# Kernel optimization log

Hardware: AMD Instinct MI355X
Metric: run time of the kernel (lower is better)

Reference implementation:

```python
import jax, jax.numpy as jnp
import numpy as np

N, E, D, L = 50000, 600000, 128, 4
SCALE = 0.05  # small init so 4 sum-aggregation layers with residuals stay bounded


def setup_inputs() -> dict:
    key = jax.random.key(0)
    ks = jax.random.split(key, 6)
    x = jax.random.normal(ks[0], (N, D), dtype=jnp.float32)
    edge_index = jax.random.randint(ks[1], (2, E), 0, N, dtype=jnp.int64)
    Wn = jax.random.normal(ks[2], (L, D, D), dtype=jnp.float32) * SCALE
    Wr = jax.random.normal(ks[3], (L, D, D), dtype=jnp.float32) * SCALE
    b = jnp.zeros((L, D), dtype=jnp.float32)
    fcW = jax.random.normal(ks[4], (D, 1), dtype=jnp.float32) * SCALE
    fcb = jnp.zeros((1,), dtype=jnp.float32)
    return {"x": x, "edge_index": edge_index, "Wn": Wn, "Wr": Wr, "b": b,
            "fcW": fcW, "fcb": fcb}


def reference(x, edge_index, Wn, Wr, b, fcW, fcb):
    # AFGCN forward (eval mode: dropout is identity).
    # GraphConv (PyG, aggr='add'): out = sum_{j in N(i)} h_j @ Wn + h_i @ Wr + b
    src, dst = edge_index[0], edge_index[1]
    h0 = x
    h = x
    for l in range(L):
        agg = jax.ops.segment_sum(h[src], dst, num_segments=N)  # [N, D]
        h = jax.nn.relu(agg @ Wn[l] + h @ Wr[l] + b[l])
        h = h + h0  # residual to the input features
    return (h @ fcW + fcb).squeeze(-1)  # [N]
```

## Files before the change

kernel.cpp:

```cpp
#include <hip/hip_runtime.h>


#define D 128

using bf16x8 = __attribute__((ext_vector_type(8))) short;
using f32x4  = __attribute__((ext_vector_type(4))) float;

__device__ inline unsigned short f2b(float f) {
    union { float f; unsigned int u; } v; v.f = f;
    unsigned int u = v.u;
    u += 0x7fffu + ((u >> 16) & 1u);
    return (unsigned short)(u >> 16);
}
__device__ inline float b2f_lo(unsigned int u) { return __uint_as_float(u << 16); }
__device__ inline float b2f_hi(unsigned int u) { return __uint_as_float(u & 0xffff0000u); }

__global__ void k_zero_i32(int* __restrict__ p, int n) {
    int i = blockIdx.x * blockDim.x + threadIdx.x;
    if (i < n) p[i] = 0;
}

__global__ void k_hist(const int* __restrict__ dst, int* __restrict__ cnt, int e) {
    int i = blockIdx.x * blockDim.x + threadIdx.x;
    if (i < e) atomicAdd(&cnt[dst[i]], 1);
}

__global__ __launch_bounds__(256) void k_scan_a(const int* __restrict__ cnt,
                                                int* __restrict__ ro,
                                                int* __restrict__ bsum, int n) {
    __shared__ int s[256];
    int tid = threadIdx.x;
    int base = blockIdx.x * 1024 + tid * 4;
    int c[4];
    #pragma unroll
    for (int k = 0; k < 4; ++k) c[k] = (base + k < n) ? cnt[base + k] : 0;
    s[tid] = c[0] + c[1] + c[2] + c[3];
    __syncthreads();
    #pragma unroll
    for (int off = 1; off < 256; off <<= 1) {
        int add = (tid >= off) ? s[tid - off] : 0;
        __syncthreads();
        s[tid] += add;
        __syncthreads();
    }
    int run = (tid == 0) ? 0 : s[tid - 1];
    #pragma unroll
    for (int k = 0; k < 4; ++k) {
        if (base + k < n) ro[base + k] = run;
        run += c[k];
    }
    if (tid == 255) bsum[blockIdx.x] = s[255];
}

__global__ __launch_bounds__(64) void k_scan_b(int* __restrict__ bsum,
                                               int* __restrict__ ro, int nb, int n) {
    int tid = threadIdx.x;
    int orig = (tid < nb) ? bsum[tid] : 0;
    int v = orig;
    #pragma unroll
    for (int off = 1; off < 64; off <<= 1) {
        int u = __shfl_up(v, off, 64);
        if (tid >= off) v += u;
    }
    if (tid < nb) bsum[tid] = v - orig;
    if (tid == 63) ro[n] = v;
}

__global__ __launch_bounds__(256) void k_scan_c(int* __restrict__ ro,
                                                int* __restrict__ cur,
                                                const int* __restrict__ bsum, int n) {
    int base = blockIdx.x * 1024 + threadIdx.x * 4;
    int off = bsum[blockIdx.x];
    #pragma unroll
    for (int k = 0; k < 4; ++k) {
        int i = base + k;
        if (i < n) { int v = ro[i] + off; ro[i] = v; cur[i] = v; }
    }
}

__global__ void k_scatter(const int* __restrict__ src, const int* __restrict__ dst,
                          int* __restrict__ cur, int* __restrict__ ssrc, int e) {
    int i = blockIdx.x * blockDim.x + threadIdx.x;
    if (i < e) {
        int pos = atomicAdd(&cur[dst[i]], 1);
        ssrc[pos] = src[i];
    }
}

__global__ void k_cvt(const float* __restrict__ in, unsigned short* __restrict__ out,
                      int n8) {
    int i = blockIdx.x * blockDim.x + threadIdx.x;
    if (i >= n8) return;
    float4 a = ((const float4*)in)[i * 2];
    float4 b = ((const float4*)in)[i * 2 + 1];
    ushort4 o0, o1;
    o0.x = f2b(a.x); o0.y = f2b(a.y); o0.z = f2b(a.z); o0.w = f2b(a.w);
    o1.x = f2b(b.x); o1.y = f2b(b.y); o1.z = f2b(b.z); o1.w = f2b(b.w);
    ((ushort4*)out)[i * 2] = o0;
    ((ushort4*)out)[i * 2 + 1] = o1;
}

__global__ void k_pack_B(const float* __restrict__ Wn, const float* __restrict__ Wr,
                         unsigned short* __restrict__ Bp) {
    int t = blockIdx.x * blockDim.x + threadIdx.x;
    int lane = t & 63;
    int nb = (t >> 6) & 7;
    int ks = (t >> 9) & 7;
    int l  = t >> 12;
    int ncol = nb * 16 + (lane & 15);
    int k0 = ks * 32 + (lane >> 4) * 8;
    ushort4 lo, hi;
    unsigned short v[8];
    #pragma unroll
    for (int j = 0; j < 8; ++j) {
        int k = k0 + j;
        float f = (k < D) ? Wn[(size_t)l * D * D + k * D + ncol]
                          : Wr[(size_t)l * D * D + (k - D) * D + ncol];
        v[j] = f2b(f);
    }
    lo.x = v[0]; lo.y = v[1]; lo.z = v[2]; lo.w = v[3];
    hi.x = v[4]; hi.y = v[5]; hi.z = v[6]; hi.w = v[7];
    ((ushort4*)Bp)[t * 2] = lo;
    ((ushort4*)Bp)[t * 2 + 1] = hi;
}

template<bool LAST>
__global__ __launch_bounds__(256) void k_fused(
        const unsigned short* __restrict__ hb,
        const int* __restrict__ ro,
        const int* __restrict__ ssrc,
        const unsigned short* __restrict__ Bp,
        const float* __restrict__ bias,
        const float* __restrict__ x0,
        unsigned short* __restrict__ hb_out,
        const float* __restrict__ fcW,
        const float* __restrict__ fcb,
        float* __restrict__ out, int n) {
    __shared__ unsigned short tsh[4][16][132];
    int wid = threadIdx.x >> 6;
    int lane = threadIdx.x & 63;
    int row0 = (blockIdx.x * 4 + wid) * 16;
    if (row0 >= n) return;

    int r = lane & 15;
    int g = lane >> 4;
    int row = row0 + r;

    float agg[4][8];
    #pragma unroll
    for (int ks = 0; ks < 4; ++ks)
        #pragma unroll
        for (int t = 0; t < 8; ++t) agg[ks][t] = 0.f;

    int s = ro[row], e = ro[row + 1];
    const unsigned short* hbg = hb + g * 8;
    for (int j = s; j < e; ++j) {
        const unsigned short* srcp = hbg + (size_t)ssrc[j] * D;
        uint4 v0 = *(const uint4*)(srcp);
        uint4 v1 = *(const uint4*)(srcp + 32);
        uint4 v2 = *(const uint4*)(srcp + 64);
        uint4 v3 = *(const uint4*)(srcp + 96);
        agg[0][0] += b2f_lo(v0.x); agg[0][1] += b2f_hi(v0.x);
        agg[0][2] += b2f_lo(v0.y); agg[0][3] += b2f_hi(v0.y);
        agg[0][4] += b2f_lo(v0.z); agg[0][5] += b2f_hi(v0.z);
        agg[0][6] += b2f_lo(v0.w); agg[0][7] += b2f_hi(v0.w);
        agg[1][0] += b2f_lo(v1.x); agg[1][1] += b2f_hi(v1.x);
        agg[1][2] += b2f_lo(v1.y); agg[1][3] += b2f_hi(v1.y);
        agg[1][4] += b2f_lo(v1.z); agg[1][5] += b2f_hi(v1.z);
        agg[1][6] += b2f_lo(v1.w); agg[1][7] += b2f_hi(v1.w);
        agg[2][0] += b2f_lo(v2.x); agg[2][1] += b2f_hi(v2.x);
        agg[2][2] += b2f_lo(v2.y); agg[2][3] += b2f_hi(v2.y);
        agg[2][4] += b2f_lo(v2.z); agg[2][5] += b2f_hi(v2.z);
        agg[2][6] += b2f_lo(v2.w); agg[2][7] += b2f_hi(v2.w);
        agg[3][0] += b2f_lo(v3.x); agg[3][1] += b2f_hi(v3.x);
        agg[3][2] += b2f_lo(v3.y); agg[3][3] += b2f_hi(v3.y);
        agg[3][4] += b2f_lo(v3.z); agg[3][5] += b2f_hi(v3.z);
        agg[3][6] += b2f_lo(v3.w); agg[3][7] += b2f_hi(v3.w);
    }

    f32x4 acc[8];
    #pragma unroll
    for (int i = 0; i < 8; ++i) {
        acc[i][0] = 0.f; acc[i][1] = 0.f; acc[i][2] = 0.f; acc[i][3] = 0.f;
    }
    const bf16x8* bp = (const bf16x8*)Bp;

    #pragma unroll
    for (int ks = 0; ks < 4; ++ks) {
        unsigned short af[8];
        #pragma unroll
        for (int t = 0; t < 8; ++t) af[t] = f2b(agg[ks][t]);
        bf16x8 afrag = *(const bf16x8*)af;
        #pragma unroll
        for (int nb = 0; nb < 8; ++nb) {
            bf16x8 bfrag = bp[(ks * 8 + nb) * 64 + lane];
            acc[nb] = __builtin_amdgcn_mfma_f32_16x16x32_bf16(afrag, bfrag, acc[nb], 0, 0, 0);
        }
    }
    const unsigned short* hrow = hb + (size_t)row * D;
    #pragma unroll
    for (int ks = 4; ks < 8; ++ks) {
        bf16x8 afrag = *(const bf16x8*)(hrow + (ks - 4) * 32 + g * 8);
        #pragma unroll
        for (int nb = 0; nb < 8; ++nb) {
            bf16x8 bfrag = bp[(ks * 8 + nb) * 64 + lane];
            acc[nb] = __builtin_amdgcn_mfma_f32_16x16x32_bf16(afrag, bfrag, acc[nb], 0, 0, 0);
        }
    }

    if (!LAST) {
        #pragma unroll
        for (int nb = 0; nb < 8; ++nb) {
            int col = nb * 16 + r;
            float bc = bias[col];
            #pragma unroll
            for (int reg = 0; reg < 4; ++reg) {
                int rowc = row0 + g * 4 + reg;
                float xv = x0[(size_t)rowc * D + col];
                float hv = fmaxf(acc[nb][reg] + bc, 0.f) + xv;
                tsh[wid][g * 4 + reg][col] = f2b(hv);
            }
        }
        #pragma unroll
        for (int it = 0; it < 4; ++it) {
            int rr = it * 4 + g;
            uint4 v = *(const uint4*)&tsh[wid][rr][r * 8];
            *(uint4*)(hb_out + (size_t)(row0 + rr) * D + r * 8) = v;
        }
    } else {
        float p[4] = {0.f, 0.f, 0.f, 0.f};
        #pragma unroll
        for (int nb = 0; nb < 8; ++nb) {
            int col = nb * 16 + r;
            float bc = bias[col];
            float fw = fcW[col];
            #pragma unroll
            for (int reg = 0; reg < 4; ++reg) {
                int rowc = row0 + g * 4 + reg;
                float xv = x0[(size_t)rowc * D + col];
                p[reg] += (fmaxf(acc[nb][reg] + bc, 0.f) + xv) * fw;
            }
        }
        #pragma unroll
        for (int reg = 0; reg < 4; ++reg) {
            #pragma unroll
            for (int m = 1; m < 16; m <<= 1) p[reg] += __shfl_xor(p[reg], m, 64);
        }
        if (r == 0) {
            float fb = fcb[0];
            #pragma unroll
            for (int reg = 0; reg < 4; ++reg) out[row0 + g * 4 + reg] = p[reg] + fb;
        }
    }
}

extern "C" void kernel_launch(void* const* d_in, const int* in_sizes, int n_in,
                              void* d_out, int out_size, void* d_ws, size_t ws_size,
                              hipStream_t stream) {
    const float* x    = (const float*)d_in[0];
    const int*   ei   = (const int*)d_in[1];
    const float* Wn   = (const float*)d_in[2];
    const float* Wr   = (const float*)d_in[3];
    const float* bias = (const float*)d_in[4];
    const float* fcW  = (const float*)d_in[5];
    const float* fcb  = (const float*)d_in[6];
    float* out = (float*)d_out;

    const int n = in_sizes[0] / D;
    const int e = in_sizes[1] / 2;

    const int* src = ei;
    const int* dst = ei + e;

    char* ws = (char*)d_ws;
    unsigned short* xb   = (unsigned short*)ws;  ws += (size_t)n * D * 2;
    unsigned short* hb_a = (unsigned short*)ws;  ws += (size_t)n * D * 2;
    unsigned short* hb_b = (unsigned short*)ws;  ws += (size_t)n * D * 2;
    unsigned short* Bp   = (unsigned short*)ws;  ws += (size_t)4 * 8 * 8 * 64 * 8 * 2;
    int* ro   = (int*)ws;  ws += (size_t)(n + 1) * 4;
    int* cur  = (int*)ws;  ws += (size_t)n * 4;
    int* ssrc = (int*)ws;  ws += (size_t)e * 4;
    int* bsum = (int*)ws;  ws += 256 * 4;
    (void)ws_size;

    const int nscan = (n + 1023) / 1024;

    k_zero_i32<<<(n + 255) / 256, 256, 0, stream>>>(cur, n);
    k_hist<<<(e + 255) / 256, 256, 0, stream>>>(dst, cur, e);
    k_scan_a<<<nscan, 256, 0, stream>>>(cur, ro, bsum, n);
    k_scan_b<<<1, 64, 0, stream>>>(bsum, ro, nscan, n);
    k_scan_c<<<nscan, 256, 0, stream>>>(ro, cur, bsum, n);
    k_scatter<<<(e + 255) / 256, 256, 0, stream>>>(src, dst, cur, ssrc, e);

    int n8 = n * D / 8;
    k_cvt<<<(n8 + 255) / 256, 256, 0, stream>>>(x, xb, n8);
    k_pack_B<<<(4 * 8 * 8 * 64) / 256, 256, 0, stream>>>(Wn, Wr, Bp);

    const int layer_blocks = ((n + 15) / 16 + 3) / 4;
    const size_t bpl = (size_t)8 * 8 * 64 * 8;

    k_fused<false><<<layer_blocks, 256, 0, stream>>>(xb, ro, ssrc, Bp,
            bias, x, hb_a, fcW, fcb, out, n);
    k_fused<false><<<layer_blocks, 256, 0, stream>>>(hb_a, ro, ssrc, Bp + bpl,
            bias + D, x, hb_b, fcW, fcb, out, n);
    k_fused<false><<<layer_blocks, 256, 0, stream>>>(hb_b, ro, ssrc, Bp + 2 * bpl,
            bias + 2 * D, x, hb_a, fcW, fcb, out, n);
    k_fused<true><<<layer_blocks, 256, 0, stream>>>(hb_a, ro, ssrc, Bp + 3 * bpl,
            bias + 3 * D, x, hb_b, fcW, fcb, out, n);
}
```

Before: 249.6 us.

## Sort nodes by degree for load balance, unroll gather, read residual as bf16

```diff
diff --git a/kernel.cpp b/kernel.cpp
--- a/kernel.cpp
+++ b/kernel.cpp
@@ -14,6 +14,11 @@
 }
 __device__ inline float b2f_lo(unsigned int u) { return __uint_as_float(u << 16); }
 __device__ inline float b2f_hi(unsigned int u) { return __uint_as_float(u & 0xffff0000u); }
+__device__ inline unsigned int badd2(unsigned int a, unsigned int b) {
+    unsigned short lo = f2b(b2f_lo(a) + b2f_lo(b));
+    unsigned short hi = f2b(b2f_hi(a) + b2f_hi(b));
+    return (unsigned int)lo | ((unsigned int)hi << 16);
+}
 
 __global__ void k_zero_i32(int* __restrict__ p, int n) {
     int i = blockIdx.x * blockDim.x + threadIdx.x;
@@ -84,6 +89,37 @@
     if (i < e) {
         int pos = atomicAdd(&cur[dst[i]], 1);
         ssrc[pos] = src[i];
+    }
+}
+
+__global__ void k_deg_hist(const int* __restrict__ ro, int* __restrict__ bh, int n) {
+    int i = blockIdx.x * blockDim.x + threadIdx.x;
+    if (i < n) {
+        int d = min(ro[i + 1] - ro[i], 63);
+        atomicAdd(&bh[d], 1);
+    }
+}
+
+__global__ __launch_bounds__(64) void k_bin_scan(const int* __restrict__ bh,
+                                                 int* __restrict__ bcur) {
+    int t = threadIdx.x;
+    int h = bh[t];
+    int v = h;
+    #pragma unroll
+    for (int off = 1; off < 64; off <<= 1) {
+        int u = __shfl_down(v, off, 64);
+        if (t + off < 64) v += u;
+    }
+    bcur[t] = v - h;
+}
+
+__global__ void k_bin_scatter(const int* __restrict__ ro, int* __restrict__ bcur,
+                              int* __restrict__ perm, int n) {
+    int i = blockIdx.x * blockDim.x + threadIdx.x;
+    if (i < n) {
+        int d = min(ro[i + 1] - ro[i], 63);
+        int pos = atomicAdd(&bcur[d], 1);
+        perm[pos] = i;
     }
 }
 
@@ -124,14 +160,21 @@
     ((ushort4*)Bp)[t * 2 + 1] = hi;
 }
 
+#define ACC8(V, KS) do { \
+    agg[KS][0] += b2f_lo((V).x); agg[KS][1] += b2f_hi((V).x); \
+    agg[KS][2] += b2f_lo((V).y); agg[KS][3] += b2f_hi((V).y); \
+    agg[KS][4] += b2f_lo((V).z); agg[KS][5] += b2f_hi((V).z); \
+    agg[KS][6] += b2f_lo((V).w); agg[KS][7] += b2f_hi((V).w); } while (0)
+
 template<bool LAST>
 __global__ __launch_bounds__(256) void k_fused(
         const unsigned short* __restrict__ hb,
         const int* __restrict__ ro,
         const int* __restrict__ ssrc,
+        const int* __restrict__ perm,
         const unsigned short* __restrict__ Bp,
         const float* __restrict__ bias,
-        const float* __restrict__ x0,
+        const unsigned short* __restrict__ xb,
         unsigned short* __restrict__ hb_out,
         const float* __restrict__ fcW,
         const float* __restrict__ fcb,
@@ -144,7 +187,7 @@
 
     int r = lane & 15;
     int g = lane >> 4;
-    int row = row0 + r;
+    int prow = perm[row0 + r];
 
     float agg[4][8];
     #pragma unroll
@@ -152,30 +195,42 @@
         #pragma unroll
         for (int t = 0; t < 8; ++t) agg[ks][t] = 0.f;
 
-    int s = ro[row], e = ro[row + 1];
+    int s = ro[prow], e = ro[prow + 1];
     const unsigned short* hbg = hb + g * 8;
-    for (int j = s; j < e; ++j) {
-        const unsigned short* srcp = hbg + (size_t)ssrc[j] * D;
-        uint4 v0 = *(const uint4*)(srcp);
-        uint4 v1 = *(const uint4*)(srcp + 32);
-        uint4 v2 = *(const uint4*)(srcp + 64);
-        uint4 v3 = *(const uint4*)(srcp + 96);
-        agg[0][0] += b2f_lo(v0.x); agg[0][1] += b2f_hi(v0.x);
-        agg[0][2] += b2f_lo(v0.y); agg[0][3] += b2f_hi(v0.y);
-        agg[0][4] += b2f_lo(v0.z); agg[0][5] += b2f_hi(v0.z);
-        agg[0][6] += b2f_lo(v0.w); agg[0][7] += b2f_hi(v0.w);
-        agg[1][0] += b2f_lo(v1.x); agg[1][1] += b2f_hi(v1.x);
-        agg[1][2] += b2f_lo(v1.y); agg[1][3] += b2f_hi(v1.y);
-        agg[1][4] += b2f_lo(v1.z); agg[1][5] += b2f_hi(v1.z);
-        agg[1][6] += b2f_lo(v1.w); agg[1][7] += b2f_hi(v1.w);
-        agg[2][0] += b2f_lo(v2.x); agg[2][1] += b2f_hi(v2.x);
-        agg[2][2] += b2f_lo(v2.y); agg[2][3] += b2f_hi(v2.y);
-        agg[2][4] += b2f_lo(v2.z); agg[2][5] += b2f_hi(v2.z);
-        agg[2][6] += b2f_lo(v2.w); agg[2][7] += b2f_hi(v2.w);
-        agg[3][0] += b2f_lo(v3.x); agg[3][1] += b2f_hi(v3.x);
-        agg[3][2] += b2f_lo(v3.y); agg[3][3] += b2f_hi(v3.y);
-        agg[3][4] += b2f_lo(v3.z); agg[3][5] += b2f_hi(v3.z);
-        agg[3][6] += b2f_lo(v3.w); agg[3][7] += b2f_hi(v3.w);
+    int j = s;
+    for (; j + 3 < e; j += 4) {
+        const unsigned short* p0 = hbg + (size_t)ssrc[j] * D;
+        const unsigned short* p1 = hbg + (size_t)ssrc[j + 1] * D;
+        const unsigned short* p2 = hbg + (size_t)ssrc[j + 2] * D;
+        const unsigned short* p3 = hbg + (size_t)ssrc[j + 3] * D;
+        uint4 a0 = *(const uint4*)(p0);
+        uint4 a1 = *(const uint4*)(p0 + 32);
+        uint4 a2 = *(const uint4*)(p0 + 64);
+        uint4 a3 = *(const uint4*)(p0 + 96);
+        uint4 b0 = *(const uint4*)(p1);
+        uint4 b1 = *(const uint4*)(p1 + 32);
+        uint4 b2 = *(const uint4*)(p1 + 64);
+        uint4 b3 = *(const uint4*)(p1 + 96);
+        uint4 c0 = *(const uint4*)(p2);
+        uint4 c1 = *(const uint4*)(p2 + 32);
+        uint4 c2 = *(const uint4*)(p2 + 64);
+        uint4 c3 = *(const uint4*)(p2 + 96);
+        uint4 d0 = *(const uint4*)(p3);
+        uint4 d1 = *(const uint4*)(p3 + 32);
+        uint4 d2 = *(const uint4*)(p3 + 64);
+        uint4 d3 = *(const uint4*)(p3 + 96);
+        ACC8(a0, 0); ACC8(a1, 1); ACC8(a2, 2); ACC8(a3, 3);
+        ACC8(b0, 0); ACC8(b1, 1); ACC8(b2, 2); ACC8(b3, 3);
+        ACC8(c0, 0); ACC8(c1, 1); ACC8(c2, 2); ACC8(c3, 3);
+        ACC8(d0, 0); ACC8(d1, 1); ACC8(d2, 2); ACC8(d3, 3);
+    }
+    for (; j < e; ++j) {
+        const unsigned short* p0 = hbg + (size_t)ssrc[j] * D;
+        uint4 a0 = *(const uint4*)(p0);
+        uint4 a1 = *(const uint4*)(p0 + 32);
+        uint4 a2 = *(const uint4*)(p0 + 64);
+        uint4 a3 = *(const uint4*)(p0 + 96);
+        ACC8(a0, 0); ACC8(a1, 1); ACC8(a2, 2); ACC8(a3, 3);
     }
 
     f32x4 acc[8];
@@ -197,7 +252,7 @@
             acc[nb] = __builtin_amdgcn_mfma_f32_16x16x32_bf16(afrag, bfrag, acc[nb], 0, 0, 0);
         }
     }
-    const unsigned short* hrow = hb + (size_t)row * D;
+    const unsigned short* hrow = hb + (size_t)prow * D;
     #pragma unroll
     for (int ks = 4; ks < 8; ++ks) {
         bf16x8 afrag = *(const bf16x8*)(hrow + (ks - 4) * 32 + g * 8);
@@ -208,48 +263,53 @@
         }
     }
 
+    #pragma unroll
+    for (int nb = 0; nb < 8; ++nb) {
+        int col = nb * 16 + r;
+        float bc = bias[col];
+        #pragma unroll
+        for (int reg = 0; reg < 4; ++reg) {
+            tsh[wid][g * 4 + reg][col] = f2b(fmaxf(acc[nb][reg] + bc, 0.f));
+        }
+    }
+
     if (!LAST) {
-        #pragma unroll
-        for (int nb = 0; nb < 8; ++nb) {
-            int col = nb * 16 + r;
-            float bc = bias[col];
-            #pragma unroll
-            for (int reg = 0; reg < 4; ++reg) {
-                int rowc = row0 + g * 4 + reg;
-                float xv = x0[(size_t)rowc * D + col];
-                float hv = fmaxf(acc[nb][reg] + bc, 0.f) + xv;
-                tsh[wid][g * 4 + reg][col] = f2b(hv);
-            }
-        }
         #pragma unroll
         for (int it = 0; it < 4; ++it) {
             int rr = it * 4 + g;
-            uint4 v = *(const uint4*)&tsh[wid][rr][r * 8];
-            *(uint4*)(hb_out + (size_t)(row0 + rr) * D + r * 8) = v;
+            int orow = perm[row0 + rr];
+            uint4 tv = *(const uint4*)&tsh[wid][rr][r * 8];
+            uint4 xv = *(const uint4*)(xb + (size_t)orow * D + r * 8);
+            uint4 o;
+            o.x = badd2(tv.x, xv.x);
+            o.y = badd2(tv.y, xv.y);
+            o.z = badd2(tv.z, xv.z);
+            o.w = badd2(tv.w, xv.w);
+            *(uint4*)(hb_out + (size_t)orow * D + r * 8) = o;
         }
     } else {
-        float p[4] = {0.f, 0.f, 0.f, 0.f};
-        #pragma unroll
-        for (int nb = 0; nb < 8; ++nb) {
-            int col = nb * 16 + r;
-            float bc = bias[col];
-            float fw = fcW[col];
+        float fw8[8];
+        *(float4*)&fw8[0] = *(const float4*)&fcW[r * 8];
+        *(float4*)&fw8[4] = *(const float4*)&fcW[r * 8 + 4];
+        float fb = fcb[0];
+        #pragma unroll
+        for (int it = 0; it < 4; ++it) {
+            int rr = it * 4 + g;
+            int orow = perm[row0 + rr];
+            uint4 tv = *(const uint4*)&tsh[wid][rr][r * 8];
+            uint4 xv = *(const uint4*)(xb + (size_t)orow * D + r * 8);
+            float p;
+            p  = (b2f_lo(tv.x) + b2f_lo(xv.x)) * fw8[0];
+            p += (b2f_hi(tv.x) + b2f_hi(xv.x)) * fw8[1];
+            p += (b2f_lo(tv.y) + b2f_lo(xv.y)) * fw8[2];
+            p += (b2f_hi(tv.y) + b2f_hi(xv.y)) * fw8[3];
+            p += (b2f_lo(tv.z) + b2f_lo(xv.z)) * fw8[4];
+            p += (b2f_hi(tv.z) + b2f_hi(xv.z)) * fw8[5];
+            p += (b2f_lo(tv.w) + b2f_lo(xv.w)) * fw8[6];
+            p += (b2f_hi(tv.w) + b2f_hi(xv.w)) * fw8[7];
             #pragma unroll
-            for (int reg = 0; reg < 4; ++reg) {
-                int rowc = row0 + g * 4 + reg;
-                float xv = x0[(size_t)rowc * D + col];
-                p[reg] += (fmaxf(acc[nb][reg] + bc, 0.f) + xv) * fw;
-            }
-        }
-        #pragma unroll
-        for (int reg = 0; reg < 4; ++reg) {
-            #pragma unroll
-            for (int m = 1; m < 16; m <<= 1) p[reg] += __shfl_xor(p[reg], m, 64);
-        }
-        if (r == 0) {
-            float fb = fcb[0];
-            #pragma unroll
-            for (int reg = 0; reg < 4; ++reg) out[row0 + g * 4 + reg] = p[reg] + fb;
+            for (int m = 1; m < 16; m <<= 1) p += __shfl_xor(p, m, 64);
+            if (r == 0) out[orow] = p + fb;
         }
     }
 }
@@ -281,6 +341,9 @@
     int* cur  = (int*)ws;  ws += (size_t)n * 4;
     int* ssrc = (int*)ws;  ws += (size_t)e * 4;
     int* bsum = (int*)ws;  ws += 256 * 4;
+    int* perm = (int*)ws;  ws += (size_t)n * 4;
+    int* bh   = (int*)ws;  ws += 64 * 4;
+    int* bcur = (int*)ws;  ws += 64 * 4;
     (void)ws_size;
 
     const int nscan = (n + 1023) / 1024;
@@ -292,6 +355,11 @@
     k_scan_c<<<nscan, 256, 0, stream>>>(ro, cur, bsum, n);
     k_scatter<<<(e + 255) / 256, 256, 0, stream>>>(src, dst, cur, ssrc, e);
 
+    k_zero_i32<<<1, 64, 0, stream>>>(bh, 64);
+    k_deg_hist<<<(n + 255) / 256, 256, 0, stream>>>(ro, bh, n);
+    k_bin_scan<<<1, 64, 0, stream>>>(bh, bcur);
+    k_bin_scatter<<<(n + 255) / 256, 256, 0, stream>>>(ro, bcur, perm, n);
+
     int n8 = n * D / 8;
     k_cvt<<<(n8 + 255) / 256, 256, 0, stream>>>(x, xb, n8);
     k_pack_B<<<(4 * 8 * 8 * 64) / 256, 256, 0, stream>>>(Wn, Wr, Bp);
@@ -299,12 +367,12 @@
     const int layer_blocks = ((n + 15) / 16 + 3) / 4;
     const size_t bpl = (size_t)8 * 8 * 64 * 8;
 
-    k_fused<false><<<layer_blocks, 256, 0, stream>>>(xb, ro, ssrc, Bp,
-            bias, x, hb_a, fcW, fcb, out, n);
-    k_fused<false><<<layer_blocks, 256, 0, stream>>>(hb_a, ro, ssrc, Bp + bpl,
-            bias + D, x, hb_b, fcW, fcb, out, n);
-    k_fused<false><<<layer_blocks, 256, 0, stream>>>(hb_b, ro, ssrc, Bp + 2 * bpl,
-            bias + 2 * D, x, hb_a, fcW, fcb, out, n);
-    k_fused<true><<<layer_blocks, 256, 0, stream>>>(hb_a, ro, ssrc, Bp + 3 * bpl,
-            bias + 3 * D, x, hb_b, fcW, fcb, out, n);
-}
+    k_fused<false><<<layer_blocks, 256, 0, stream>>>(xb, ro, ssrc, perm, Bp,
+            bias, xb, hb_a, fcW, fcb, out, n);
+    k_fused<false><<<layer_blocks, 256, 0, stream>>>(hb_a, ro, ssrc, perm, Bp + bpl,
+            bias + D, xb, hb_b, fcW, fcb, out, n);
+    k_fused<false><<<layer_blocks, 256, 0, stream>>>(hb_b, ro, ssrc, perm, Bp + 2 * bpl,
+            bias + 2 * D, xb, hb_a, fcW, fcb, out, n);
+    k_fused<true><<<layer_blocks, 256, 0, stream>>>(hb_a, ro, ssrc, perm, Bp + 3 * bpl,
+            bias + 3 * D, xb, hb_b, fcW, fcb, out, n);
+}
```

Result: slower. 542.3 us (+117.3%).
